# Kernel tuning notes

Hardware: AMD Instinct MI355X
Metric: run time of the kernel (lower is better)

The kernel has to match this reference:

```python
import jax, jax.numpy as jnp
import numpy as np

N = 100000
E = 1600000
NFEAT = 128
NHID = 16
HEADS = 4
NCLASS = 40
NEG_SLOPE = 0.2
BN_EPS = 1e-5


def setup_inputs() -> dict:
    key = jax.random.key(0)
    ks = jax.random.split(key, 16)
    HC = NHID * HEADS  # 64
    x = jax.random.normal(ks[0], (N, NFEAT), dtype=jnp.float32)
    edge_index = jax.random.randint(ks[1], (2, E), 0, N, dtype=jnp.int64)
    def glorot(k, shape, fan_in):
        return jax.random.normal(k, shape, dtype=jnp.float32) * (1.0 / np.sqrt(fan_in))
    return {
        "x": x,
        "edge_index": edge_index,
        # layer 1: GATConv(NFEAT -> NHID, heads=HEADS, concat=True)
        "W1": glorot(ks[2], (NFEAT, HC), NFEAT),
        "att_src1": glorot(ks[3], (HEADS, NHID), NHID),
        "att_dst1": glorot(ks[4], (HEADS, NHID), NHID),
        "bias1": jnp.zeros((HC,), dtype=jnp.float32),
        # BatchNorm1d(HC), eval mode (running stats)
        "bn_gamma": jnp.ones((HC,), dtype=jnp.float32),
        "bn_beta": jnp.zeros((HC,), dtype=jnp.float32),
        "bn_mean": jax.random.normal(ks[5], (HC,), dtype=jnp.float32) * 0.1,
        "bn_var": jax.random.uniform(ks[6], (HC,), dtype=jnp.float32, minval=0.5, maxval=1.5),
        # layer 2: GATConv(HC -> NCLASS, heads=1, concat=False)
        "W2": glorot(ks[7], (HC, NCLASS), HC),
        "att_src2": glorot(ks[8], (1, NCLASS), NCLASS),
        "att_dst2": glorot(ks[9], (1, NCLASS), NCLASS),
        "bias2": jnp.zeros((NCLASS,), dtype=jnp.float32),
    }


def gat_conv(x, src, dst, W, att_src, att_dst, bias, concat):
    """PyG GATConv (eval; self-loops assumed already appended to src/dst)."""
    H, C = att_src.shape
    n = x.shape[0]
    h = (x @ W).reshape(n, H, C)                         # [N,H,C]
    a_s = (h * att_src[None]).sum(-1)                    # [N,H]
    a_d = (h * att_dst[None]).sum(-1)                    # [N,H]
    alpha = jax.nn.leaky_relu(a_s[src] + a_d[dst], NEG_SLOPE)  # [Et,H]
    # segment softmax over incoming edges of each destination node
    amax = jax.ops.segment_max(alpha, dst, num_segments=n)    # [N,H]
    ex = jnp.exp(alpha - amax[dst])
    denom = jax.ops.segment_sum(ex, dst, num_segments=n)
    coef = ex / denom[dst]                               # [Et,H]
    msg = h[src] * coef[:, :, None]                      # [Et,H,C]
    out = jax.ops.segment_sum(msg, dst, num_segments=n)  # [N,H,C]
    out = out.reshape(n, H * C) if concat else out.mean(axis=1)
    return out + bias


def reference(x, edge_index, W1, att_src1, att_dst1, bias1,
              bn_gamma, bn_beta, bn_mean, bn_var,
              W2, att_src2, att_dst2, bias2):
    n = x.shape[0]
    loops = jnp.arange(n, dtype=edge_index.dtype)
    src = jnp.concatenate([edge_index[0], loops])
    dst = jnp.concatenate([edge_index[1], loops])
    h = gat_conv(x, src, dst, W1, att_src1, att_dst1, bias1, concat=True)
    h = (h - bn_mean) * jax.lax.rsqrt(bn_var + BN_EPS) * bn_gamma + bn_beta
    h = jax.nn.relu(h)  # dropout is identity in eval
    out = gat_conv(h, src, dst, W2, att_src2, att_dst2, bias2, concat=False)
    return out
```

## Files before the change

kernel.cpp:

```cpp
#include <hip/hip_runtime.h>
#include <hip/hip_bf16.h>
#include <hip/hip_fp16.h>

#define NFEAT  128
#define HC     64
#define HEADS  4
#define NHID   16
#define NCLASS 40
#define NEG    0.2f
#define BN_EPS 1e-5f

#define BK_SH   9
#define CHUNK   8192
#define STAGE   12288

typedef _Float16 half8_t __attribute__((ext_vector_type(8)));
typedef _Float16 half4_t __attribute__((ext_vector_type(4)));
typedef float    f32x4_t __attribute__((ext_vector_type(4)));

__device__ __forceinline__ float leaky(float a) { return (a > 0.f) ? a : NEG * a; }

__global__ __launch_bounds__(256) void k_gemm1(
    const float* __restrict__ x, const float* __restrict__ W1,
    const float* __restrict__ att_s, const float* __restrict__ att_d,
    __half* __restrict__ h1, float* __restrict__ as1, float* __restrict__ ad1,
    int n)
{
    const int wave = threadIdx.x >> 6, lane = threadIdx.x & 63;
    const int quad = lane >> 4, l16 = lane & 15;

    half8_t bfrag[4][4];
    #pragma unroll
    for (int ks = 0; ks < 4; ++ks)
        #pragma unroll
        for (int ct = 0; ct < 4; ++ct)
            #pragma unroll
            for (int j = 0; j < 8; ++j)
                bfrag[ks][ct][j] =
                    (_Float16)W1[(ks * 32 + quad * 8 + j) * HC + ct * 16 + l16];

    float avs[4], avd[4];
    #pragma unroll
    for (int ct = 0; ct < 4; ++ct) {
        avs[ct] = att_s[ct * 16 + l16];
        avd[ct] = att_d[ct * 16 + l16];
    }

    const int nslab = (n + 15) >> 4;
    for (int slab = blockIdx.x * 4 + wave; slab < nslab; slab += gridDim.x * 4) {
        const int rowbase = slab * 16;
        const int arow = min(rowbase + l16, n - 1);
        const float* xp = x + (size_t)arow * NFEAT;

        f32x4_t acc[4] = {{0.f,0.f,0.f,0.f},{0.f,0.f,0.f,0.f},
                          {0.f,0.f,0.f,0.f},{0.f,0.f,0.f,0.f}};
        #pragma unroll
        for (int ks = 0; ks < 4; ++ks) {
            const float4 xa = *(const float4*)(xp + ks * 32 + quad * 8);
            const float4 xb = *(const float4*)(xp + ks * 32 + quad * 8 + 4);
            half8_t af;
            af[0] = (_Float16)xa.x; af[1] = (_Float16)xa.y;
            af[2] = (_Float16)xa.z; af[3] = (_Float16)xa.w;
            af[4] = (_Float16)xb.x; af[5] = (_Float16)xb.y;
            af[6] = (_Float16)xb.z; af[7] = (_Float16)xb.w;
            #pragma unroll
            for (int ct = 0; ct < 4; ++ct)
                acc[ct] = __builtin_amdgcn_mfma_f32_16x16x32_f16(
                    af, bfrag[ks][ct], acc[ct], 0, 0, 0);
        }

        #pragma unroll
        for (int reg = 0; reg < 4; ++reg) {
            const int row = rowbase + quad * 4 + reg;
            const bool valid = row < n;

            float4 ps, pd;
            ps.x = acc[0][reg] * avs[0]; pd.x = acc[0][reg] * avd[0];
            ps.y = acc[1][reg] * avs[1]; pd.y = acc[1][reg] * avd[1];
            ps.z = acc[2][reg] * avs[2]; pd.z = acc[2][reg] * avd[2];
            ps.w = acc[3][reg] * avs[3]; pd.w = acc[3][reg] * avd[3];
            #pragma unroll
            for (int off = 8; off >= 1; off >>= 1) {
                ps.x += __shfl_xor(ps.x, off, 64); pd.x += __shfl_xor(pd.x, off, 64);
                ps.y += __shfl_xor(ps.y, off, 64); pd.y += __shfl_xor(pd.y, off, 64);
                ps.z += __shfl_xor(ps.z, off, 64); pd.z += __shfl_xor(pd.z, off, 64);
                ps.w += __shfl_xor(ps.w, off, 64); pd.w += __shfl_xor(pd.w, off, 64);
            }
            if (valid) {
                #pragma unroll
                for (int ct = 0; ct < 4; ++ct)
                    h1[(size_t)row * HC + ct * 16 + l16] =
                        __float2half_rn(acc[ct][reg]);
                if (l16 == 0) {
                    *(float4*)(as1 + (size_t)row * HEADS) = ps;
                    *(float4*)(ad1 + (size_t)row * HEADS) = pd;
                }
            }
        }
    }
}

__global__ __launch_bounds__(512) void k_hist(
    const int* __restrict__ edst, int* __restrict__ hist, int E, int nbk)
{
    __shared__ int lh[256];
    const int w = blockIdx.x, t = threadIdx.x;
    for (int i = t; i < nbk; i += 512) lh[i] = 0;
    __syncthreads();
    const int lo = w * CHUNK, hi = min(E, lo + CHUNK);
    for (int e = lo + 4 * t; e < hi; e += 4 * 512) {
        const int4 d4 = *(const int4*)(edst + e);
        atomicAdd(&lh[d4.x >> BK_SH], 1);
        atomicAdd(&lh[d4.y >> BK_SH], 1);
        atomicAdd(&lh[d4.z >> BK_SH], 1);
        atomicAdd(&lh[d4.w >> BK_SH], 1);
    }
    __syncthreads();
    for (int i = t; i < nbk; i += 512) hist[(size_t)w * nbk + i] = lh[i];
}

__global__ __launch_bounds__(256) void k_colscan(
    int* __restrict__ hist, int* __restrict__ colsum, int nbk, int nw)
{
    __shared__ int wred[4];
    const int b = blockIdx.x, t = threadIdx.x;
    const int lane = t & 63, w = t >> 6;
    const int v = (t < nw) ? hist[(size_t)t * nbk + b] : 0;
    int sc = v;
    #pragma unroll
    for (int off = 1; off < 64; off <<= 1) {
        int u = __shfl_up(sc, off, 64);
        if (lane >= off) sc += u;
    }
    if (lane == 63) wred[w] = sc;
    __syncthreads();
    if (t == 0) { int a = 0; for (int i = 0; i < 4; ++i) { int xx = wred[i]; wred[i] = a; a += xx; } }
    __syncthreads();
    const int excl = sc - v + wred[w];
    if (t < nw) hist[(size_t)t * nbk + b] = excl;
    if (t == nw - 1) colsum[b] = excl + v;
}

__global__ __launch_bounds__(256) void k_bscan(
    const int* __restrict__ colsum, int* __restrict__ bstart, int nbk, int E)
{
    __shared__ int wred[4];
    const int t = threadIdx.x, lane = t & 63, w = t >> 6;
    const int v = (t < nbk) ? colsum[t] : 0;
    int sc = v;
    #pragma unroll
    for (int off = 1; off < 64; off <<= 1) {
        int u = __shfl_up(sc, off, 64);
        if (lane >= off) sc += u;
    }
    if (lane == 63) wred[w] = sc;
    __syncthreads();
    if (t == 0) { int a = 0; for (int i = 0; i < 4; ++i) { int xx = wred[i]; wred[i] = a; a += xx; } }
    __syncthreads();
    if (t < nbk) bstart[t] = sc - v + wred[w];
    if (t == 0) bstart[nbk] = E;
}

__global__ __launch_bounds__(512) void k_scatter(
    const int* __restrict__ esrc, const int* __restrict__ edst,
    const int* __restrict__ hist, const int* __restrict__ bstart,
    int2* __restrict__ pairs, int E, int nbk)
{
    __shared__ int cur[256];
    const int w = blockIdx.x, t = threadIdx.x;
    for (int i = t; i < nbk; i += 512)
        cur[i] = bstart[i] + hist[(size_t)w * nbk + i];
    __syncthreads();
    const int lo = w * CHUNK, hi = min(E, lo + CHUNK);
    for (int e = lo + 4 * t; e < hi; e += 4 * 512) {
        const int4 s4 = *(const int4*)(esrc + e);
        const int4 d4 = *(const int4*)(edst + e);
        int pos;
        pos = atomicAdd(&cur[d4.x >> BK_SH], 1); pairs[pos] = make_int2(s4.x, d4.x);
        pos = atomicAdd(&cur[d4.y >> BK_SH], 1); pairs[pos] = make_int2(s4.y, d4.y);
        pos = atomicAdd(&cur[d4.z >> BK_SH], 1); pairs[pos] = make_int2(s4.z, d4.z);
        pos = atomicAdd(&cur[d4.w >> BK_SH], 1); pairs[pos] = make_int2(s4.w, d4.w);
    }
}

__global__ __launch_bounds__(512) void k_build(
    const int2* __restrict__ pairs, const int* __restrict__ bstart,
    int* __restrict__ rowptr, int* __restrict__ csr, int n, int nbk)
{
    __shared__ int cnt[512];
    __shared__ int cur[512];
    __shared__ int stage[STAGE];
    __shared__ int wred[8];
    const int b = blockIdx.x, t = threadIdx.x;
    const int base = bstart[b], eend = bstart[b + 1], m = eend - base;
    const int n0 = b << BK_SH;
    const int nn = min(512, n - n0);

    cnt[t] = 0;
    __syncthreads();
    for (int e = base + t; e < eend; e += 512)
        atomicAdd(&cnt[pairs[e].y - n0], 1);
    __syncthreads();

    const int v = cnt[t];
    const int lane = t & 63, w = t >> 6;
    int sc = v;
    #pragma unroll
    for (int off = 1; off < 64; off <<= 1) {
        int u = __shfl_up(sc, off, 64);
        if (lane >= off) sc += u;
    }
    if (lane == 63) wred[w] = sc;
    __syncthreads();
    if (t == 0) { int a = 0; for (int i = 0; i < 8; ++i) { int xx = wred[i]; wred[i] = a; a += xx; } }
    __syncthreads();
    const int excl = sc - v + wred[w];
    cur[t] = excl;
    if (t < nn) rowptr[n0 + t] = base + excl + v;
    __syncthreads();

    for (int e = base + t; e < eend; e += 512) {
        const int2 p = pairs[e];
        const int loc = atomicAdd(&cur[p.y - n0], 1);
        if (loc < STAGE) stage[loc] = p.x;
        else             csr[base + loc] = p.x;
    }
    __syncthreads();
    const int lim = min(m, STAGE);
    for (int i = t; i < lim; i += 512) csr[base + i] = stage[i];
}

__global__ __launch_bounds__(256, 4) void k_agg1(
    const int* __restrict__ csr, const int* __restrict__ rowptr,
    const __half* __restrict__ h1, const float* __restrict__ as1,
    const float* __restrict__ ad1,
    const float* __restrict__ bias1, const float* __restrict__ gamma,
    const float* __restrict__ beta, const float* __restrict__ mean,
    const float* __restrict__ var,
    const float* __restrict__ W2, const float* __restrict__ ats2,
    const float* __restrict__ atd2,
    __half* __restrict__ g, float* __restrict__ as2o, float* __restrict__ ad2o,
    int n)
{
    __shared__ _Float16 sWh[NCLASS * HC];
    __shared__ float sh[16][68];
    __shared__ float sE[16][4][20];
    __shared__ int   sS[16][20];
    for (int i = threadIdx.x; i < NCLASS * HC; i += 256) sWh[i] = (_Float16)W2[i];
    __syncthreads();

    const int gi = threadIdx.x >> 4;
    const int q  = threadIdx.x & 15;
    const int myh = q >> 2;

    const float4 b1v = *(const float4*)(bias1 + 4 * q);
    const float4 gmv = *(const float4*)(gamma + 4 * q);
    const float4 vrv = *(const float4*)(var   + 4 * q);
    const float4 mnv = *(const float4*)(mean  + 4 * q);
    const float4 btv = *(const float4*)(beta  + 4 * q);
    float4 scv, shv;
    scv.x = gmv.x * rsqrtf(vrv.x + BN_EPS);
    scv.y = gmv.y * rsqrtf(vrv.y + BN_EPS);
    scv.z = gmv.z * rsqrtf(vrv.z + BN_EPS);
    scv.w = gmv.w * rsqrtf(vrv.w + BN_EPS);
    shv.x = btv.x - mnv.x * scv.x;
    shv.y = btv.y - mnv.y * scv.y;
    shv.z = btv.z - mnv.z * scv.z;
    shv.w = btv.w - mnv.w * scv.w;
    float4 at2 = {0.f, 0.f, 0.f, 0.f}, dt2 = {0.f, 0.f, 0.f, 0.f};
    if (q < 10) {
        at2 = *(const float4*)(ats2 + 4 * q);
        dt2 = *(const float4*)(atd2 + 4 * q);
    }

    for (int node0 = blockIdx.x * 16; node0 < n; node0 += gridDim.x * 16) {
        const int node = node0 + gi;
        if (node >= n) continue;

        const float4 adv = *(const float4*)(ad1 + node * HEADS);
        const float4 sv4 = *(const float4*)(as1 + node * HEADS);
        float4 eself;
        eself.x = __expf(leaky(sv4.x + adv.x));
        eself.y = __expf(leaky(sv4.y + adv.y));
        eself.z = __expf(leaky(sv4.z + adv.z));
        eself.w = __expf(leaky(sv4.w + adv.w));
        const float es = (myh == 0) ? eself.x : (myh == 1) ? eself.y
                       : (myh == 2) ? eself.z : eself.w;

        {
            const half4_t hv = *(const half4_t*)(h1 + (size_t)node * HC + 4 * q);
            float4 a;
            a.x = es * (float)hv[0]; a.y = es * (float)hv[1];
            a.z = es * (float)hv[2]; a.w = es * (float)hv[3];
            *(float4*)&sh[gi][4 * q] = a;
        }
        float4 acc = *(float4*)&sh[gi][4 * q];
        float4 dpart = {0.f, 0.f, 0.f, 0.f};

        const int start = (node == 0) ? 0 : rowptr[node - 1];
        const int end   = rowptr[node];

        if (start < end) {
            int ia = csr[min(start + q, end - 1)];
            for (int base = start; base < end; base += 16) {
                const int m = end - base;

                const float4 s4 = *(const float4*)(as1 + (size_t)ia * HEADS);
                const int ia_next = csr[min(base + 16 + q, end - 1)];

                sS[gi][q] = ia;

                int idxs[16];
                *(int4*)&idxs[0]  = *(const int4*)&sS[gi][0];
                *(int4*)&idxs[4]  = *(const int4*)&sS[gi][4];
                *(int4*)&idxs[8]  = *(const int4*)&sS[gi][8];
                *(int4*)&idxs[12] = *(const int4*)&sS[gi][12];

                half4_t wreg[16];
                #pragma unroll
                for (int e = 0; e < 16; ++e) {
                    const unsigned off = ((unsigned)idxs[e] << 7) + ((unsigned)q << 3);
                    wreg[e] = *(const half4_t*)((const char*)h1 + off);
                }
                __builtin_amdgcn_sched_barrier(0);

                const bool val = q < m;
                float4 ea;
                ea.x = val ? __expf(leaky(s4.x + adv.x)) : 0.f;
                ea.y = val ? __expf(leaky(s4.y + adv.y)) : 0.f;
                ea.z = val ? __expf(leaky(s4.z + adv.z)) : 0.f;
                ea.w = val ? __expf(leaky(s4.w + adv.w)) : 0.f;
                dpart.x += ea.x; dpart.y += ea.y;
                dpart.z += ea.z; dpart.w += ea.w;
                sE[gi][0][q] = ea.x;
                sE[gi][1][q] = ea.y;
                sE[gi][2][q] = ea.z;
                sE[gi][3][q] = ea.w;

                float eev[16];
                *(float4*)&eev[0]  = *(const float4*)&sE[gi][myh][0];
                *(float4*)&eev[4]  = *(const float4*)&sE[gi][myh][4];
                *(float4*)&eev[8]  = *(const float4*)&sE[gi][myh][8];
                *(float4*)&eev[12] = *(const float4*)&sE[gi][myh][12];

                #pragma unroll
                for (int e = 0; e < 16; ++e) {
                    const float ee = eev[e];
                    acc.x = fmaf((float)wreg[e][0], ee, acc.x);
                    acc.y = fmaf((float)wreg[e][1], ee, acc.y);
                    acc.z = fmaf((float)wreg[e][2], ee, acc.z);
                    acc.w = fmaf((float)wreg[e][3], ee, acc.w);
                }
                ia = ia_next;
            }
        }

        #pragma unroll
        for (int off = 8; off >= 1; off >>= 1) {
            dpart.x += __shfl_xor(dpart.x, off, 64);
            dpart.y += __shfl_xor(dpart.y, off, 64);
            dpart.z += __shfl_xor(dpart.z, off, 64);
            dpart.w += __shfl_xor(dpart.w, off, 64);
        }
        const float den = es + ((myh == 0) ? dpart.x : (myh == 1) ? dpart.y
                               : (myh == 2) ? dpart.z : dpart.w);
        const float rden = 1.f / den;

        float4 v;
        v.x = fmaxf(fmaf(acc.x * rden + b1v.x, scv.x, shv.x), 0.f);
        v.y = fmaxf(fmaf(acc.y * rden + b1v.y, scv.y, shv.y), 0.f);
        v.z = fmaxf(fmaf(acc.z * rden + b1v.z, scv.z, shv.z), 0.f);
        v.w = fmaxf(fmaf(acc.w * rden + b1v.w, scv.w, shv.w), 0.f);
        *(float4*)&sh[gi][4 * q] = v;

        float4 gacc = {0.f, 0.f, 0.f, 0.f};
        if (q < 10) {
            #pragma unroll 8
            for (int k = 0; k < HC; ++k) {
                const float hk = sh[gi][k];
                const half4_t wv = *(const half4_t*)&sWh[k * NCLASS + 4 * q];
                gacc.x = fmaf(hk, (float)wv[0], gacc.x);
                gacc.y = fmaf(hk, (float)wv[1], gacc.y);
                gacc.z = fmaf(hk, (float)wv[2], gacc.z);
                gacc.w = fmaf(hk, (float)wv[3], gacc.w);
            }
        }
        __half2 p0 = __float22half2_rn({gacc.x, gacc.y});
        __half2 p1 = __float22half2_rn({gacc.z, gacc.w});
        float2 packed; *(__half2*)&packed.x = p0; *(__half2*)&packed.y = p1;
        *(float2*)(g + (size_t)node * HC + 4 * q) = packed;

        float sv = gacc.x * at2.x + gacc.y * at2.y + gacc.z * at2.z + gacc.w * at2.w;
        float dv = gacc.x * dt2.x + gacc.y * dt2.y + gacc.z * dt2.z + gacc.w * dt2.w;
        #pragma unroll
        for (int off = 8; off >= 1; off >>= 1) {
            sv += __shfl_xor(sv, off, 64);
            dv += __shfl_xor(dv, off, 64);
        }
        if (q == 0) { as2o[node] = sv; ad2o[node] = dv; }
    }
}

__global__ __launch_bounds__(256, 4) void k_agg2(
    const int* __restrict__ csr, const int* __restrict__ rowptr,
    const __half* __restrict__ g, const float* __restrict__ as2,
    const float* __restrict__ ad2, const float* __restrict__ bias2,
    float* __restrict__ out, int n)
{
    __shared__ float sE[16][20];
    __shared__ int   sS[16][20];
    const int gi = threadIdx.x >> 4;
    const int q  = threadIdx.x & 15;

    float4 b2v = {0.f, 0.f, 0.f, 0.f};
    if (q < 10) b2v = *(const float4*)(bias2 + 4 * q);

    for (int node0 = blockIdx.x * 16; node0 < n; node0 += gridDim.x * 16) {
        const int node = node0 + gi;
        if (node >= n) continue;

        const float ad2d = ad2[node];
        const float eself = __expf(leaky(as2[node] + ad2d));

        float4 acc;
        {
            const half4_t hv = *(const half4_t*)(g + (size_t)node * HC + 4 * q);
            acc.x = eself * (float)hv[0]; acc.y = eself * (float)hv[1];
            acc.z = eself * (float)hv[2]; acc.w = eself * (float)hv[3];
        }
        float dpart = 0.f;

        const int start = (node == 0) ? 0 : rowptr[node - 1];
        const int end   = rowptr[node];

        if (start < end) {
            int ia = csr[min(start + q, end - 1)];
            for (int base = start; base < end; base += 16) {
                const int m = end - base;

                const float sca = as2[ia];
                const int ia_next = csr[min(base + 16 + q, end - 1)];

                sS[gi][q] = ia;

                int idxs[16];
                *(int4*)&idxs[0]  = *(const int4*)&sS[gi][0];
                *(int4*)&idxs[4]  = *(const int4*)&sS[gi][4];
                *(int4*)&idxs[8]  = *(const int4*)&sS[gi][8];
                *(int4*)&idxs[12] = *(const int4*)&sS[gi][12];

                half4_t wreg[16];
                #pragma unroll
                for (int e = 0; e < 16; ++e) {
                    const unsigned off = ((unsigned)idxs[e] << 7) + ((unsigned)q << 3);
                    wreg[e] = *(const half4_t*)((const char*)g + off);
                }
                __builtin_amdgcn_sched_barrier(0);

                const float ea = (q < m) ? __expf(leaky(sca + ad2d)) : 0.f;
                dpart += ea;
                sE[gi][q] = ea;

                float eev[16];
                *(float4*)&eev[0]  = *(const float4*)&sE[gi][0];
                *(float4*)&eev[4]  = *(const float4*)&sE[gi][4];
                *(float4*)&eev[8]  = *(const float4*)&sE[gi][8];
                *(float4*)&eev[12] = *(const float4*)&sE[gi][12];

                #pragma unroll
                for (int e = 0; e < 16; ++e) {
                    const float ee = eev[e];
                    acc.x = fmaf((float)wreg[e][0], ee, acc.x);
                    acc.y = fmaf((float)wreg[e][1], ee, acc.y);
                    acc.z = fmaf((float)wreg[e][2], ee, acc.z);
                    acc.w = fmaf((float)wreg[e][3], ee, acc.w);
                }
                ia = ia_next;
            }
        }

        #pragma unroll
        for (int off = 8; off >= 1; off >>= 1)
            dpart += __shfl_xor(dpart, off, 64);
        const float rden = 1.f / (dpart + eself);

        if (q < 10) {
            float4 r;
            r.x = acc.x * rden + b2v.x;
            r.y = acc.y * rden + b2v.y;
            r.z = acc.z * rden + b2v.z;
            r.w = acc.w * rden + b2v.w;
            *(float4*)(out + (size_t)node * NCLASS + 4 * q) = r;
        }
    }
}

extern "C" void kernel_launch(void* const* d_in, const int* in_sizes, int n_in,
                              void* d_out, int out_size, void* d_ws, size_t ws_size,
                              hipStream_t stream)
{
    const float* x    = (const float*)d_in[0];
    const int*   ei   = (const int*)  d_in[1];
    const float* W1   = (const float*)d_in[2];
    const float* as1w = (const float*)d_in[3];
    const float* ad1w = (const float*)d_in[4];
    const float* b1   = (const float*)d_in[5];
    const float* gm   = (const float*)d_in[6];
    const float* bt   = (const float*)d_in[7];
    const float* mn   = (const float*)d_in[8];
    const float* vr   = (const float*)d_in[9];
    const float* W2   = (const float*)d_in[10];
    const float* as2w = (const float*)d_in[11];
    const float* ad2w = (const float*)d_in[12];
    const float* b2   = (const float*)d_in[13];

    const int n = in_sizes[0] / NFEAT;
    const int E = in_sizes[1] / 2;
    const int* esrc = ei;
    const int* edst = ei + E;

    const int nbk = (n + 511) >> BK_SH;
    const int nw  = (E + CHUNK - 1) / CHUNK;

    float*  ws   = (float*)d_ws;
    __half* h1   = (__half*)ws;
    float*  a_s1 = ws   + (size_t)n * 32;
    float*  a_d1 = a_s1 + (size_t)n * 4;
    __half* gbuf = (__half*)(a_d1 + (size_t)n * 4);
    float*  a_s2 = a_d1 + (size_t)n * 4 + (size_t)n * 32;
    float*  a_d2 = a_s2 + n;
    int2*   pairs  = (int2*)(a_d2 + n);
    int*    csr    = (int*)(pairs + E);
    int*    rowptr = csr + E;
    int*    hist   = rowptr + n;
    int*    colsum = hist + (size_t)nw * nbk;
    int*    bstart = colsum + nbk;
    float*  outv = (float*)d_out;

    const int nblk = (n + 15) / 16;

    k_hist   <<<nw, 512, 0, stream>>>(edst, hist, E, nbk);
    k_colscan<<<nbk, 256, 0, stream>>>(hist, colsum, nbk, nw);
    k_bscan  <<<1, 256, 0, stream>>>(colsum, bstart, nbk, E);
    k_scatter<<<nw, 512, 0, stream>>>(esrc, edst, hist, bstart, pairs, E, nbk);
    k_build  <<<nbk, 512, 0, stream>>>(pairs, bstart, rowptr, csr, n, nbk);
    k_gemm1  <<<512, 256, 0, stream>>>(x, W1, as1w, ad1w, h1, a_s1, a_d1, n);
    k_agg1   <<<nblk, 256, 0, stream>>>(csr, rowptr, h1, a_s1, a_d1,
                                        b1, gm, bt, mn, vr,
                                        W2, as2w, ad2w, gbuf, a_s2, a_d2, n);
    k_agg2   <<<nblk, 256, 0, stream>>>(csr, rowptr, gbuf, a_s2, a_d2,
                                        b2, outv, n);
}
```

Before: 263.3 us.

## Load CSR neighbor indices directly per lane and use persistent grid for aggregation

The aggregation kernels drop the LDS broadcast of neighbor indices and the software-prefetched next-chunk index. Each lane now reads all 16 indices of the chunk straight from the CSR array (a uniform, cached load), clamping out-of-range indices so overreads past the segment stay in bounds. The launch grid for both aggregation kernels becomes a fixed 2048 blocks that grid-stride over nodes instead of one block per 16 nodes. The LDS staging through sh for the self term is also removed. This trades LDS traffic and a barrier-like dependency for redundant global/L1 index loads and loses the cross-iteration index prefetch.

```diff
diff --git a/kernel.cpp b/kernel.cpp
--- a/kernel.cpp
+++ b/kernel.cpp
@@ -245,13 +245,13 @@
     __shared__ _Float16 sWh[NCLASS * HC];
     __shared__ float sh[16][68];
     __shared__ float sE[16][4][20];
-    __shared__ int   sS[16][20];
     for (int i = threadIdx.x; i < NCLASS * HC; i += 256) sWh[i] = (_Float16)W2[i];
     __syncthreads();
 
     const int gi = threadIdx.x >> 4;
     const int q  = threadIdx.x & 15;
     const int myh = q >> 2;
+    const unsigned nclamp = (unsigned)(n - 1);
 
     const float4 b1v = *(const float4*)(bias1 + 4 * q);
     const float4 gmv = *(const float4*)(gamma + 4 * q);
@@ -287,71 +287,63 @@
         const float es = (myh == 0) ? eself.x : (myh == 1) ? eself.y
                        : (myh == 2) ? eself.z : eself.w;
 
+        float4 acc;
         {
             const half4_t hv = *(const half4_t*)(h1 + (size_t)node * HC + 4 * q);
-            float4 a;
-            a.x = es * (float)hv[0]; a.y = es * (float)hv[1];
-            a.z = es * (float)hv[2]; a.w = es * (float)hv[3];
-            *(float4*)&sh[gi][4 * q] = a;
-        }
-        float4 acc = *(float4*)&sh[gi][4 * q];
+            acc.x = es * (float)hv[0]; acc.y = es * (float)hv[1];
+            acc.z = es * (float)hv[2]; acc.w = es * (float)hv[3];
+        }
         float4 dpart = {0.f, 0.f, 0.f, 0.f};
 
         const int start = (node == 0) ? 0 : rowptr[node - 1];
         const int end   = rowptr[node];
 
-        if (start < end) {
-            int ia = csr[min(start + q, end - 1)];
-            for (int base = start; base < end; base += 16) {
-                const int m = end - base;
-
-                const float4 s4 = *(const float4*)(as1 + (size_t)ia * HEADS);
-                const int ia_next = csr[min(base + 16 + q, end - 1)];
-
-                sS[gi][q] = ia;
-
-                int idxs[16];
-                *(int4*)&idxs[0]  = *(const int4*)&sS[gi][0];
-                *(int4*)&idxs[4]  = *(const int4*)&sS[gi][4];
-                *(int4*)&idxs[8]  = *(const int4*)&sS[gi][8];
-                *(int4*)&idxs[12] = *(const int4*)&sS[gi][12];
-
-                half4_t wreg[16];
-                #pragma unroll
-                for (int e = 0; e < 16; ++e) {
-                    const unsigned off = ((unsigned)idxs[e] << 7) + ((unsigned)q << 3);
-                    wreg[e] = *(const half4_t*)((const char*)h1 + off);
-                }
-                __builtin_amdgcn_sched_barrier(0);
-
-                const bool val = q < m;
-                float4 ea;
-                ea.x = val ? __expf(leaky(s4.x + adv.x)) : 0.f;
-                ea.y = val ? __expf(leaky(s4.y + adv.y)) : 0.f;
-                ea.z = val ? __expf(leaky(s4.z + adv.z)) : 0.f;
-                ea.w = val ? __expf(leaky(s4.w + adv.w)) : 0.f;
-                dpart.x += ea.x; dpart.y += ea.y;
-                dpart.z += ea.z; dpart.w += ea.w;
-                sE[gi][0][q] = ea.x;
-                sE[gi][1][q] = ea.y;
-                sE[gi][2][q] = ea.z;
-                sE[gi][3][q] = ea.w;
-
-                float eev[16];
-                *(float4*)&eev[0]  = *(const float4*)&sE[gi][myh][0];
-                *(float4*)&eev[4]  = *(const float4*)&sE[gi][myh][4];
-                *(float4*)&eev[8]  = *(const float4*)&sE[gi][myh][8];
-                *(float4*)&eev[12] = *(const float4*)&sE[gi][myh][12];
-
-                #pragma unroll
-                for (int e = 0; e < 16; ++e) {
-                    const float ee = eev[e];
-                    acc.x = fmaf((float)wreg[e][0], ee, acc.x);
-                    acc.y = fmaf((float)wreg[e][1], ee, acc.y);
-                    acc.z = fmaf((float)wreg[e][2], ee, acc.z);
-                    acc.w = fmaf((float)wreg[e][3], ee, acc.w);
-                }
-                ia = ia_next;
+        for (int base = start; base < end; base += 16) {
+            const int m = end - base;
+            const int* cb = csr + base;
+
+            const int myraw = cb[min(q, m - 1)];
+            int idxs[16];
+            #pragma unroll
+            for (int e = 0; e < 16; ++e) idxs[e] = cb[e];
+
+            half4_t wreg[16];
+            #pragma unroll
+            for (int e = 0; e < 16; ++e) {
+                const unsigned off =
+                    (min((unsigned)idxs[e], nclamp) << 7) + ((unsigned)q << 3);
+                wreg[e] = *(const half4_t*)((const char*)h1 + off);
+            }
+            const float4 s4 =
+                *(const float4*)(as1 + (size_t)min((unsigned)myraw, nclamp) * HEADS);
+            __builtin_amdgcn_sched_barrier(0);
+
+            const bool val = q < m;
+            float4 ea;
+            ea.x = val ? __expf(leaky(s4.x + adv.x)) : 0.f;
+            ea.y = val ? __expf(leaky(s4.y + adv.y)) : 0.f;
+            ea.z = val ? __expf(leaky(s4.z + adv.z)) : 0.f;
+            ea.w = val ? __expf(leaky(s4.w + adv.w)) : 0.f;
+            dpart.x += ea.x; dpart.y += ea.y;
+            dpart.z += ea.z; dpart.w += ea.w;
+            sE[gi][0][q] = ea.x;
+            sE[gi][1][q] = ea.y;
+            sE[gi][2][q] = ea.z;
+            sE[gi][3][q] = ea.w;
+
+            float eev[16];
+            *(float4*)&eev[0]  = *(const float4*)&sE[gi][myh][0];
+            *(float4*)&eev[4]  = *(const float4*)&sE[gi][myh][4];
+            *(float4*)&eev[8]  = *(const float4*)&sE[gi][myh][8];
+            *(float4*)&eev[12] = *(const float4*)&sE[gi][myh][12];
+
+            #pragma unroll
+            for (int e = 0; e < 16; ++e) {
+                const float ee = eev[e];
+                acc.x = fmaf((float)wreg[e][0], ee, acc.x);
+                acc.y = fmaf((float)wreg[e][1], ee, acc.y);
+                acc.z = fmaf((float)wreg[e][2], ee, acc.z);
+                acc.w = fmaf((float)wreg[e][3], ee, acc.w);
             }
         }
 
@@ -408,9 +400,9 @@
     float* __restrict__ out, int n)
 {
     __shared__ float sE[16][20];
-    __shared__ int   sS[16][20];
     const int gi = threadIdx.x >> 4;
     const int q  = threadIdx.x & 15;
+    const unsigned nclamp = (unsigned)(n - 1);
 
     float4 b2v = {0.f, 0.f, 0.f, 0.f};
     if (q < 10) b2v = *(const float4*)(bias2 + 4 * q);
@@ -433,49 +425,42 @@
         const int start = (node == 0) ? 0 : rowptr[node - 1];
         const int end   = rowptr[node];
 
-        if (start < end) {
-            int ia = csr[min(start + q, end - 1)];
-            for (int base = start; base < end; base += 16) {
-                const int m = end - base;
-
-                const float sca = as2[ia];
-                const int ia_next = csr[min(base + 16 + q, end - 1)];
-
-                sS[gi][q] = ia;
-
-                int idxs[16];
-                *(int4*)&idxs[0]  = *(const int4*)&sS[gi][0];
-                *(int4*)&idxs[4]  = *(const int4*)&sS[gi][4];
-                *(int4*)&idxs[8]  = *(const int4*)&sS[gi][8];
-                *(int4*)&idxs[12] = *(const int4*)&sS[gi][12];
-
-                half4_t wreg[16];
-                #pragma unroll
-                for (int e = 0; e < 16; ++e) {
-                    const unsigned off = ((unsigned)idxs[e] << 7) + ((unsigned)q << 3);
-                    wreg[e] = *(const half4_t*)((const char*)g + off);
-                }
-                __builtin_amdgcn_sched_barrier(0);
-
-                const float ea = (q < m) ? __expf(leaky(sca + ad2d)) : 0.f;
-                dpart += ea;
-                sE[gi][q] = ea;
-
-                float eev[16];
-                *(float4*)&eev[0]  = *(const float4*)&sE[gi][0];
-                *(float4*)&eev[4]  = *(const float4*)&sE[gi][4];
-                *(float4*)&eev[8]  = *(const float4*)&sE[gi][8];
-                *(float4*)&eev[12] = *(const float4*)&sE[gi][12];
-
-                #pragma unroll
-                for (int e = 0; e < 16; ++e) {
-                    const float ee = eev[e];
-                    acc.x = fmaf((float)wreg[e][0], ee, acc.x);
-                    acc.y = fmaf((float)wreg[e][1], ee, acc.y);
-                    acc.z = fmaf((float)wreg[e][2], ee, acc.z);
-                    acc.w = fmaf((float)wreg[e][3], ee, acc.w);
-                }
-                ia = ia_next;
+        for (int base = start; base < end; base += 16) {
+            const int m = end - base;
+            const int* cb = csr + base;
+
+            const int myraw = cb[min(q, m - 1)];
+            int idxs[16];
+            #pragma unroll
+            for (int e = 0; e < 16; ++e) idxs[e] = cb[e];
+
+            half4_t wreg[16];
+            #pragma unroll
+            for (int e = 0; e < 16; ++e) {
+                const unsigned off =
+                    (min((unsigned)idxs[e], nclamp) << 7) + ((unsigned)q << 3);
+                wreg[e] = *(const half4_t*)((const char*)g + off);
+            }
+            const float sca = as2[min((unsigned)myraw, nclamp)];
+            __builtin_amdgcn_sched_barrier(0);
+
+            const float ea = (q < m) ? __expf(leaky(sca + ad2d)) : 0.f;
+            dpart += ea;
+            sE[gi][q] = ea;
+
+            float eev[16];
+            *(float4*)&eev[0]  = *(const float4*)&sE[gi][0];
+            *(float4*)&eev[4]  = *(const float4*)&sE[gi][4];
+            *(float4*)&eev[8]  = *(const float4*)&sE[gi][8];
+            *(float4*)&eev[12] = *(const float4*)&sE[gi][12];
+
+            #pragma unroll
+            for (int e = 0; e < 16; ++e) {
+                const float ee = eev[e];
+                acc.x = fmaf((float)wreg[e][0], ee, acc.x);
+                acc.y = fmaf((float)wreg[e][1], ee, acc.y);
+                acc.z = fmaf((float)wreg[e][2], ee, acc.z);
+                acc.w = fmaf((float)wreg[e][3], ee, acc.w);
             }
         }
 
@@ -537,7 +522,7 @@
     int*    bstart = colsum + nbk;
     float*  outv = (float*)d_out;
 
-    const int nblk = (n + 15) / 16;
+    const int nblk = 2048;
 
     k_hist   <<<nw, 512, 0, stream>>>(edst, hist, E, nbk);
     k_colscan<<<nbk, 256, 0, stream>>>(hist, colsum, nbk, nw);
```

Result: no change. 265.6 us (+0.9%).
